# Optimization experiments

Measured on AMD Instinct MI355X. Metric: run time of the kernel, lower is better.

Reference implementation:

```python
import jax, jax.numpy as jnp
import numpy as np

B, N, D, V = 512, 200, 128, 100000

def setup_inputs() -> dict:
    key = jax.random.key(0)
    ks = jax.random.split(key, 13)
    s = 1.0 / np.sqrt(D)
    return {
        "x": jax.random.randint(ks[0], (B, N), 0, V),
        "A": jax.random.uniform(ks[1], (B, N, 2 * N), dtype=jnp.float32),
        "emb": jax.random.normal(ks[2], (V, D), dtype=jnp.float32) * s,
        "w_in": jax.random.normal(ks[3], (D, D), dtype=jnp.float32) * s,
        "b_in": jax.random.normal(ks[4], (D,), dtype=jnp.float32) * s,
        "w_out": jax.random.normal(ks[5], (D, D), dtype=jnp.float32) * s,
        "b_out": jax.random.normal(ks[6], (D,), dtype=jnp.float32) * s,
        "w_ih": jax.random.normal(ks[7], (3 * D, 2 * D), dtype=jnp.float32) * s,
        "b_ih": jax.random.normal(ks[8], (3 * D,), dtype=jnp.float32) * s,
        "w_hh": jax.random.normal(ks[9], (3 * D, D), dtype=jnp.float32) * s,
        "b_hh": jax.random.normal(ks[10], (3 * D,), dtype=jnp.float32) * s,
        "b_iah": jax.random.normal(ks[11], (D,), dtype=jnp.float32) * s,
        "b_oah": jax.random.normal(ks[12], (D,), dtype=jnp.float32) * s,
    }

def reference(x, A, emb, w_in, b_in, w_out, b_out, w_ih, b_ih, w_hh, b_hh, b_iah, b_oah):
    hidden = emb[x]                                   # [B, N, D]
    n = A.shape[1]
    # neighbor aggregation via in/out adjacency halves
    input_in = jnp.matmul(A[:, :, :n], hidden @ w_in.T + b_in) + b_iah    # [B, N, D]
    input_out = jnp.matmul(A[:, :, n:2 * n], hidden @ w_out.T + b_out) + b_oah
    inputs = jnp.concatenate([input_in, input_out], axis=2)               # [B, N, 2D]
    gi = inputs @ w_ih.T + b_ih                        # [B, N, 3D]
    gh = hidden @ w_hh.T + b_hh                        # [B, N, 3D]
    d = hidden.shape[-1]
    i_r, i_i, i_n = gi[..., :d], gi[..., d:2 * d], gi[..., 2 * d:]
    h_r, h_i, h_n = gh[..., :d], gh[..., d:2 * d], gh[..., 2 * d:]
    gate_input = jax.nn.sigmoid(i_i + h_i)
    gate_reset = jax.nn.sigmoid(i_r + h_r)
    gate_output = jnp.tanh(i_n + gate_reset * h_n)
    return gate_output + gate_input * (hidden - gate_output)
```

## Files before the change

### kernel.cpp

```cpp
#include <hip/hip_runtime.h>
#include <math.h>

#define BB 512
#define NN 200
#define DD 128
#define BNROWS (BB*NN)

typedef float f32x4 __attribute__((ext_vector_type(4)));
typedef short bf16x8 __attribute__((ext_vector_type(8)));
typedef unsigned short u16x4 __attribute__((ext_vector_type(4)));

#define MFMA16(a,b,c) __builtin_amdgcn_mfma_f32_16x16x32_bf16(a,b,c,0,0,0)

#define GLL(gp, lp) __builtin_amdgcn_global_load_lds( \
    (const __attribute__((address_space(1))) unsigned int*)(gp), \
    (__attribute__((address_space(3))) unsigned int*)(lp), 16, 0, 0)

#define KWAITV(S) asm volatile("s_waitcnt vmcnt(" S ")" ::: "memory")
#define KWAITL()  asm volatile("s_waitcnt lgkmcnt(0)" ::: "memory")
#define KBAR()    __builtin_amdgcn_s_barrier()
#define KSBAR()   __builtin_amdgcn_sched_barrier(0)

#define OFF_ZHI   ((size_t)0)
#define OFF_ZLO   (OFF_ZHI + (size_t)BNROWS*384*2)
#define OFF_HT    (OFF_ZLO + (size_t)BNROWS*256*2)
#define OFF_M1    (OFF_HT  + (size_t)BB*128*224*2)
#define OFF_M2    (OFF_M1  + (size_t)384*128*4)
#define OFF_WH    (OFF_M2  + (size_t)384*128*4)
#define OFF_WL    (OFF_WH  + (size_t)512*384*2)
#define OFF_CC    (OFF_WL  + (size_t)512*384*2)
#define OFF_U1V   (OFF_CC  + 512*4)
#define OFF_U2V   (OFF_U1V + 512*4)
#define OFF_U1    (OFF_U2V + 512*4)
#define OFF_U2    (OFF_U1  + 384*4)
#define OFF_C0    (OFF_U2  + 384*4)
#define OFF_RSI   (OFF_C0  + 384*4)
#define OFF_RSO   (OFF_RSI + (size_t)BNROWS*4)
#define WS_BYTES  (OFF_RSO + (size_t)BNROWS*4)

__device__ inline unsigned short f2bf(float x) {
  unsigned int u = __float_as_uint(x);
  unsigned int r = u + 0x7FFFu + ((u >> 16) & 1u);
  return (unsigned short)(r >> 16);
}
__device__ inline float bf2f(unsigned short h) {
  return __uint_as_float(((unsigned int)h) << 16);
}
__device__ inline float fsigmoid(float x) {
  return 1.f / (1.f + __expf(-x));
}
__device__ inline float ftanh(float x) {
  x = fminf(15.f, fmaxf(-15.f, x));
  float e = __expf(-2.f * x);
  return (1.f - e) / (1.f + e);
}

__global__ __launch_bounds__(128) void kprep(
    const float* __restrict__ w_ih, const float* __restrict__ w_in,
    const float* __restrict__ w_out, const float* __restrict__ b_in,
    const float* __restrict__ b_out, const float* __restrict__ b_iah,
    const float* __restrict__ b_oah, const float* __restrict__ b_ih,
    float* __restrict__ M1, float* __restrict__ M2,
    float* __restrict__ u1, float* __restrict__ u2, float* __restrict__ c0) {
  __shared__ float wrow[256];
  const int j = blockIdx.x;
  const int k = threadIdx.x;
  wrow[k]       = w_ih[(size_t)j * 256 + k];
  wrow[128 + k] = w_ih[(size_t)j * 256 + 128 + k];
  __syncthreads();
  float a1 = 0.f, a2 = 0.f;
  for (int t = 0; t < 128; ++t) {
    a1 = fmaf(wrow[t],       w_in[t * 128 + k],  a1);
    a2 = fmaf(wrow[128 + t], w_out[t * 128 + k], a2);
  }
  M1[j * 128 + k] = a1;
  M2[j * 128 + k] = a2;
  if (k == 0) {
    float s1 = 0.f, s2 = 0.f, s0 = 0.f;
    for (int t = 0; t < 128; ++t) {
      s1 = fmaf(wrow[t], b_in[t], s1);
      s2 = fmaf(wrow[128 + t], b_out[t], s2);
      s0 = fmaf(wrow[t], b_iah[t], s0);
      s0 = fmaf(wrow[128 + t], b_oah[t], s0);
    }
    u1[j] = s1; u2[j] = s2; c0[j] = s0 + b_ih[j];
  }
}

__global__ void wcat_build(const float* __restrict__ M1, const float* __restrict__ M2,
                           const float* __restrict__ w_hh, const float* __restrict__ b_hh,
                           const float* __restrict__ u1, const float* __restrict__ u2,
                           const float* __restrict__ c0,
                           unsigned short* __restrict__ Wh, unsigned short* __restrict__ Wl,
                           float* __restrict__ cc, float* __restrict__ u1v,
                           float* __restrict__ u2v) {
  int idx = blockIdx.x * 256 + threadIdx.x;
  if (idx >= 512 * 384) return;
  int jp = idx / 384, k = idx - jp * 384;
  int nh = jp >> 8, ng = (jp >> 7) & 1, t = (jp >> 4) & 7, q = jp & 15;
  int blk = t >> 1, s = t & 1;
  int c = nh * 64 + ng * 32 + s * 16 + q;
  int g = (blk <= 1) ? blk : 2;
  int j = g * 128 + c;
  float val;
  if (k < 128)      val = (blk == 3) ? 0.f : M1[j * 128 + k];
  else if (k < 256) val = (blk == 3) ? 0.f : M2[j * 128 + (k - 128)];
  else              val = (blk == 2) ? 0.f : w_hh[(size_t)j * 128 + (k - 256)];
  unsigned short h = f2bf(val);
  Wh[idx] = h;
  Wl[idx] = f2bf(val - bf2f(h));
  if (k == 0) {
    float ccv, a1, a2;
    if (blk == 0)      { ccv = c0[c] + b_hh[c];             a1 = u1[c];       a2 = u2[c]; }
    else if (blk == 1) { ccv = c0[128 + c] + b_hh[128 + c]; a1 = u1[128 + c]; a2 = u2[128 + c]; }
    else if (blk == 2) { ccv = c0[256 + c];                 a1 = u1[256 + c]; a2 = u2[256 + c]; }
    else               { ccv = b_hh[256 + c];               a1 = 0.f;         a2 = 0.f; }
    cc[jp] = ccv; u1v[jp] = a1; u2v[jp] = a2;
  }
}

__global__ __launch_bounds__(256) void k1_gather(
    const int* __restrict__ x, const float* __restrict__ emb,
    unsigned short* __restrict__ hT, unsigned short* __restrict__ Z_hi) {
  __shared__ float hid[32][132];
  const int t = threadIdx.x;
  const int b = blockIdx.x;
  const int m0 = blockIdx.y * 32;
  for (int i = t; i < 32 * 128; i += 256) {
    int r = i >> 7, c = i & 127;
    int m = m0 + r;
    int rowc = b * 200 + (m < 200 ? m : 199);
    float h = emb[(size_t)x[rowc] * 128 + c];
    hid[r][c] = h;
    if (m < 200) Z_hi[(size_t)(b * 200 + m) * 384 + 256 + c] = f2bf(h);
  }
  __syncthreads();
  {
    int c = t >> 1, half = t & 1;
    bf16x8 p0, p1;
    #pragma unroll
    for (int j = 0; j < 16; ++j) {
      int ml = half * 16 + j;
      bool valid = (m0 + ml) < 200;
      float fv = valid ? hid[ml][c] : 0.f;
      if (j < 8) p0[j] = (short)f2bf(fv);
      else       p1[j - 8] = (short)f2bf(fv);
    }
    size_t base = ((size_t)(b * 128 + c)) * 224 + m0 + half * 16;
    *(bf16x8*)&hT[base]     = p0;
    *(bf16x8*)&hT[base + 8] = p1;
  }
}

__global__ __launch_bounds__(256, 2) void k2_amm(
    const float* __restrict__ A, const unsigned short* __restrict__ hT,
    unsigned short* __restrict__ Z_hi, unsigned short* __restrict__ Z_lo,
    float* __restrict__ rs_in, float* __restrict__ rs_out) {
  __shared__ alignas(16) unsigned short Ainh[2][64][40];
  __shared__ alignas(16) unsigned short Ainl[2][64][40];
  __shared__ alignas(16) unsigned short Aouth[2][64][40];
  __shared__ alignas(16) unsigned short Aoutl[2][64][40];
  __shared__ alignas(16) unsigned short Bv[2][128][32];
  const int t = threadIdx.x;
  const int b = blockIdx.x;
  const int m0 = blockIdx.y * 64;
  const int wv = t >> 6, lane = t & 63;
  const int q = lane & 15, quad = lane >> 4;
  const int sel = wv >> 1, nh2 = wv & 1;
  const int lrow = lane >> 2, lseg = lane & 3;

  const int am = t >> 2, aseg = t & 3;
  const int gm = m0 + am;
  const bool mvalid = gm < 200;
  const float* arow = A + (size_t)(b * 200 + (mvalid ? gm : 199)) * 400;

  f32x4 acc[4][4];
  #pragma unroll
  for (int i = 0; i < 4; ++i)
    #pragma unroll
    for (int j = 0; j < 4; ++j) acc[i][j] = 0.f;
  float rsi = 0.f, rso = 0.f;

  #define AISSUE(K0, P0, P1, Q0, Q1) do {                                       \
    int kb_ = (K0) + aseg * 8;                                                  \
    int kc_ = (kb_ < 200) ? kb_ : 0;                                            \
    P0 = *(const f32x4*)(arow + kc_);                                           \
    P1 = *(const f32x4*)(arow + kc_ + 4);                                       \
    Q0 = *(const f32x4*)(arow + 200 + kc_);                                     \
    Q1 = *(const f32x4*)(arow + 200 + kc_ + 4);                                 \
  } while (0)

  #define STAGE_B(K0, BUF) do {                                                 \
    _Pragma("unroll")                                                           \
    for (int op_ = 0; op_ < 2; ++op_) {                                         \
      int j_ = wv * 32 + op_ * 16 + lrow;                                       \
      int c_ = ((j_ >> 6) << 6) + ((j_ & 15) << 2) + ((j_ >> 4) & 3);           \
      GLL(hT + ((size_t)(b * 128 + c_)) * 224 + (K0) + lseg * 8,                \
          &Bv[BUF][wv * 32 + op_ * 16][0]);                                     \
    }                                                                           \
  } while (0)

  #define ACONV(K0, BUF, P0, P1, Q0, Q1) do {                                   \
    bool kv_ = mvalid && ((K0) + aseg * 8 < 200);                               \
    float fin_[8], fot_[8];                                                     \
    fin_[0]=P0.x; fin_[1]=P0.y; fin_[2]=P0.z; fin_[3]=P0.w;                     \
    fin_[4]=P1.x; fin_[5]=P1.y; fin_[6]=P1.z; fin_[7]=P1.w;                     \
    fot_[0]=Q0.x; fot_[1]=Q0.y; fot_[2]=Q0.z; fot_[3]=Q0.w;                     \
    fot_[4]=Q1.x; fot_[5]=Q1.y; fot_[6]=Q1.z; fot_[7]=Q1.w;                     \
    bf16x8 ih_, il_, oh_, ol_;                                                  \
    _Pragma("unroll")                                                           \
    for (int e_ = 0; e_ < 8; ++e_) {                                            \
      float fi_ = kv_ ? fin_[e_] : 0.f;                                         \
      float fo_ = kv_ ? fot_[e_] : 0.f;                                         \
      rsi += fi_; rso += fo_;                                                   \
      unsigned short h1_ = f2bf(fi_);                                           \
      ih_[e_] = (short)h1_; il_[e_] = (short)f2bf(fi_ - bf2f(h1_));             \
      unsigned short h2_ = f2bf(fo_);                                           \
      oh_[e_] = (short)h2_; ol_[e_] = (short)f2bf(fo_ - bf2f(h2_));             \
    }                                                                           \
    *(bf16x8*)&Ainh[BUF][am][aseg * 8]  = ih_;                                  \
    *(bf16x8*)&Ainl[BUF][am][aseg * 8]  = il_;                                  \
    *(bf16x8*)&Aouth[BUF][am][aseg * 8] = oh_;                                  \
    *(bf16x8*)&Aoutl[BUF][am][aseg * 8] = ol_;                                  \
  } while (0)

  #define K2COMP(BUF) do {                                                      \
    const unsigned short (*Ath_)[40] = sel ? Aouth[BUF] : Ainh[BUF];            \
    const unsigned short (*Atl_)[40] = sel ? Aoutl[BUF] : Ainl[BUF];            \
    bf16x8 ah_[4], al_[4];                                                      \
    _Pragma("unroll")                                                           \
    for (int mt = 0; mt < 4; ++mt) {                                            \
      ah_[mt] = *(const bf16x8*)&Ath_[mt * 16 + q][quad * 8];                   \
      al_[mt] = *(const bf16x8*)&Atl_[mt * 16 + q][quad * 8];                   \
    }                                                                           \
    _Pragma("unroll")                                                           \
    for (int nt = 0; nt < 4; ++nt) {                                            \
      bf16x8 bb_ = *(const bf16x8*)&Bv[BUF][nh2 * 64 + nt * 16 + q][quad * 8];  \
      _Pragma("unroll")                                                         \
      for (int mt = 0; mt < 4; ++mt) {                                          \
        acc[mt][nt] = MFMA16(ah_[mt], bb_, acc[mt][nt]);                        \
        acc[mt][nt] = MFMA16(al_[mt], bb_, acc[mt][nt]);                        \
      }                                                                         \
    }                                                                           \
  } while (0)

  f32x4 cp0, cp1, cq0, cq1;
  AISSUE(0, cp0, cp1, cq0, cq1);
  STAGE_B(0, 0);
  int buf = 0;

  for (int k = 0; k < 6; ++k) {
    const int k0n = (k + 1) * 32;
    f32x4 np0, np1, nq0, nq1;
    AISSUE(k0n, np0, np1, nq0, nq1);
    STAGE_B(k0n, buf ^ 1);
    KWAITV("6"); KSBAR();
    ACONV(k * 32, buf, cp0, cp1, cq0, cq1);
    KWAITL(); KSBAR(); KBAR();
    K2COMP(buf);
    KBAR();
    cp0 = np0; cp1 = np1; cq0 = nq0; cq1 = nq1;
    buf ^= 1;
  }
  KWAITV("0"); KSBAR();
  ACONV(192, buf, cp0, cp1, cq0, cq1);
  KWAITL(); KSBAR(); KBAR();
  K2COMP(buf);

  const int colb = sel * 128 + nh2 * 64 + q * 4;
  #pragma unroll
  for (int mt = 0; mt < 4; ++mt) {
    #pragma unroll
    for (int r = 0; r < 4; ++r) {
      int m = m0 + mt * 16 + quad * 4 + r;
      if (m < 200) {
        u16x4 h4, l4;
        #pragma unroll
        for (int nt = 0; nt < 4; ++nt) {
          float v = acc[mt][nt][r];
          unsigned short hs = f2bf(v);
          h4[nt] = hs;
          l4[nt] = f2bf(v - bf2f(hs));
        }
        size_t row = (size_t)(b * 200 + m);
        *(u16x4*)&Z_hi[row * 384 + colb] = h4;
        *(u16x4*)&Z_lo[row * 256 + colb] = l4;
      }
    }
  }
  rsi += __shfl_xor(rsi, 1); rsi += __shfl_xor(rsi, 2);
  rso += __shfl_xor(rso, 1); rso += __shfl_xor(rso, 2);
  if (aseg == 0 && mvalid) {
    rs_in[(size_t)b * 200 + gm]  = rsi;
    rs_out[(size_t)b * 200 + gm] = rso;
  }
  #undef AISSUE
  #undef STAGE_B
  #undef ACONV
  #undef K2COMP
}

__global__ __launch_bounds__(256, 2) void k3_gates(
    const unsigned short* __restrict__ Z_hi, const unsigned short* __restrict__ Z_lo,
    const unsigned short* __restrict__ Wh, const unsigned short* __restrict__ Wl,
    const float* __restrict__ cc, const float* __restrict__ u1v,
    const float* __restrict__ u2v, const float* __restrict__ rs_in,
    const float* __restrict__ rs_out, float* __restrict__ out) {
  __shared__ alignas(16) unsigned short WhS[256][32];
  __shared__ alignas(16) unsigned short WlS[256][32];
  __shared__ alignas(16) unsigned short Ah[2][128][32];
  __shared__ alignas(16) unsigned short Al[2][128][32];
  const int t = threadIdx.x;
  const int w = t >> 6, lane = t & 63;
  const int q = lane & 15, quad = lane >> 4;
  const int mh = w >> 1, ng = w & 1;
  const int lrow = lane >> 2, lseg = lane & 3;
  const size_t rbase = (size_t)blockIdx.x * 128;
  const int nh = blockIdx.y;

  f32x4 acc[4][8];
  #pragma unroll
  for (int i = 0; i < 4; ++i)
    #pragma unroll
    for (int j = 0; j < 8; ++j) acc[i][j] = 0.f;

  #define STAGE_W(KC) do {                                                      \
    const int k0_ = (KC) * 32;                                                  \
    _Pragma("unroll")                                                           \
    for (int c_ = 0; c_ < 4; ++c_) {                                            \
      int j_ = w * 64 + c_ * 16;                                                \
      GLL(Wh + (size_t)(nh * 256 + j_ + lrow) * 384 + k0_ + lseg * 8,           \
          &WhS[j_][0]);                                                         \
    }                                                                           \
    _Pragma("unroll")                                                           \
    for (int c_ = 0; c_ < 4; ++c_) {                                            \
      int j_ = w * 64 + c_ * 16;                                                \
      GLL(Wl + (size_t)(nh * 256 + j_ + lrow) * 384 + k0_ + lseg * 8,           \
          &WlS[j_][0]);                                                         \
    }                                                                           \
  } while (0)

  #define STAGE_A1(KC, BUF) do {                                                \
    const int k0_ = (KC) * 32;                                                  \
    _Pragma("unroll")                                                           \
    for (int c_ = 0; c_ < 2; ++c_) {                                            \
      int m_ = w * 32 + c_ * 16;                                                \
      GLL(Z_hi + (rbase + m_ + lrow) * 384 + k0_ + lseg * 8, &Ah[BUF][m_][0]);  \
    }                                                                           \
    _Pragma("unroll")                                                           \
    for (int c_ = 0; c_ < 2; ++c_) {                                            \
      int m_ = w * 32 + c_ * 16;                                                \
      GLL(Z_lo + (rbase + m_ + lrow) * 256 + k0_ + lseg * 8, &Al[BUF][m_][0]);  \
    }                                                                           \
  } while (0)

  #define STAGE_A2(KC, BUF) do {                                                \
    const int k0_ = (KC) * 32;                                                  \
    _Pragma("unroll")                                                           \
    for (int c_ = 0; c_ < 2; ++c_) {                                            \
      int m_ = w * 32 + c_ * 16;                                                \
      GLL(Z_hi + (rbase + m_ + lrow) * 384 + k0_ + lseg * 8, &Ah[BUF][m_][0]);  \
    }                                                                           \
  } while (0)

  #define COMPUTE1(BUF) do {                                                    \
    bf16x8 ah_[4], al_[4];                                                      \
    _Pragma("unroll")                                                           \
    for (int mt = 0; mt < 4; ++mt) {                                            \
      ah_[mt] = *(const bf16x8*)&Ah[BUF][mh * 64 + mt * 16 + q][quad * 8];      \
      al_[mt] = *(const bf16x8*)&Al[BUF][mh * 64 + mt * 16 + q][quad * 8];      \
    }                                                                           \
    _Pragma("unroll")                                                           \
    for (int tt = 0; tt < 6; ++tt) {                                            \
      bf16x8 bh = *(const bf16x8*)&WhS[ng * 128 + tt * 16 + q][quad * 8];       \
      bf16x8 bl = *(const bf16x8*)&WlS[ng * 128 + tt * 16 + q][quad * 8];       \
      _Pragma("unroll")                                                         \
      for (int mt = 0; mt < 4; ++mt) {                                          \
        acc[mt][tt] = MFMA16(ah_[mt], bh, acc[mt][tt]);                         \
        acc[mt][tt] = MFMA16(ah_[mt], bl, acc[mt][tt]);                         \
        acc[mt][tt] = MFMA16(al_[mt], bh, acc[mt][tt]);                         \
      }                                                                         \
    }                                                                           \
  } while (0)

  #define COMPUTE2(BUF) do {                                                    \
    bf16x8 ah_[4];                                                              \
    _Pragma("unroll")                                                           \
    for (int mt = 0; mt < 4; ++mt)                                              \
      ah_[mt] = *(const bf16x8*)&Ah[BUF][mh * 64 + mt * 16 + q][quad * 8];      \
    _Pragma("unroll")                                                           \
    for (int ti = 0; ti < 6; ++ti) {                                            \
      const int tt = (ti < 4) ? ti : ti + 2;             \
      bf16x8 bh = *(const bf16x8*)&WhS[ng * 128 + tt * 16 + q][quad * 8];       \
      bf16x8 bl = *(const bf16x8*)&WlS[ng * 128 + tt * 16 + q][quad * 8];       \
      _Pragma("unroll")                                                         \
      for (int mt = 0; mt < 4; ++mt) {                                          \
        acc[mt][tt] = MFMA16(ah_[mt], bh, acc[mt][tt]);                         \
        acc[mt][tt] = MFMA16(ah_[mt], bl, acc[mt][tt]);                         \
      }                                                                         \
    }                                                                           \
  } while (0)

  STAGE_A1(0, 0);
  int buf = 0;
  #pragma unroll
  for (int kc = 0; kc < 7; ++kc) {
    STAGE_W(kc);
    STAGE_A1(kc + 1, buf ^ 1);
    KWAITV("4"); KSBAR(); KBAR();
    COMPUTE1(buf);
    KWAITL(); KSBAR(); KBAR();
    buf ^= 1;
  }
  {
    STAGE_W(7);
    STAGE_A2(8, buf ^ 1);
    KWAITV("2"); KSBAR(); KBAR();
    COMPUTE1(buf);
    KWAITL(); KSBAR(); KBAR();
    buf ^= 1;
  }
  #pragma unroll
  for (int kc = 8; kc < 11; ++kc) {
    STAGE_W(kc);
    STAGE_A2(kc + 1, buf ^ 1);
    KWAITV("2"); KSBAR(); KBAR();
    COMPUTE2(buf);
    KWAITL(); KSBAR(); KBAR();
    buf ^= 1;
  }
  {
    STAGE_W(11);
    KWAITV("0"); KSBAR(); KBAR();
    COMPUTE2(buf);
  }

  const int jb = nh * 256 + ng * 128;
  float cs[2][4], a1s[2][3], a2s[2][3];
  #pragma unroll
  for (int s = 0; s < 2; ++s) {
    #pragma unroll
    for (int gb = 0; gb < 4; ++gb) cs[s][gb] = cc[jb + (gb * 2 + s) * 16 + q];
    #pragma unroll
    for (int gb = 0; gb < 3; ++gb) {
      a1s[s][gb] = u1v[jb + (gb * 2 + s) * 16 + q];
      a2s[s][gb] = u2v[jb + (gb * 2 + s) * 16 + q];
    }
  }
  #pragma unroll
  for (int mt = 0; mt < 4; ++mt) {
    #pragma unroll
    for (int r = 0; r < 4; ++r) {
      size_t row = rbase + mh * 64 + mt * 16 + quad * 4 + r;
      float rin = rs_in[row], rot = rs_out[row];
      #pragma unroll
      for (int s = 0; s < 2; ++s) {
        int c = nh * 64 + ng * 32 + s * 16 + q;
        float sr  = acc[mt][0 + s][r] + cs[s][0] + rin * a1s[s][0] + rot * a2s[s][0];
        float si  = acc[mt][2 + s][r] + cs[s][1] + rin * a1s[s][1] + rot * a2s[s][1];
        float ani = acc[mt][4 + s][r] + cs[s][2] + rin * a1s[s][2] + rot * a2s[s][2];
        float anh = acc[mt][6 + s][r] + cs[s][3];
        float g_rs = fsigmoid(sr);
        float g_in = fsigmoid(si);
        float g_ot = ftanh(ani + g_rs * anh);
        float h = bf2f(Z_hi[row * 384 + 256 + c]);
        out[row * 128 + c] = g_ot + g_in * (h - g_ot);
      }
    }
  }
  #undef STAGE_W
  #undef STAGE_A1
  #undef STAGE_A2
  #undef COMPUTE1
  #undef COMPUTE2
}

extern "C" void kernel_launch(void* const* d_in, const int* in_sizes, int n_in,
                              void* d_out, int out_size, void* d_ws, size_t ws_size,
                              hipStream_t stream) {
  const int*   x     = (const int*)d_in[0];
  const float* A     = (const float*)d_in[1];
  const float* emb   = (const float*)d_in[2];
  const float* w_in  = (const float*)d_in[3];
  const float* b_in  = (const float*)d_in[4];
  const float* w_out = (const float*)d_in[5];
  const float* b_out = (const float*)d_in[6];
  const float* w_ih  = (const float*)d_in[7];
  const float* b_ih  = (const float*)d_in[8];
  const float* w_hh  = (const float*)d_in[9];
  const float* b_hh  = (const float*)d_in[10];
  const float* b_iah = (const float*)d_in[11];
  const float* b_oah = (const float*)d_in[12];
  float* out = (float*)d_out;
  char* ws = (char*)d_ws;

  if (ws_size < WS_BYTES) return;

  unsigned short* Z_hi = (unsigned short*)(ws + OFF_ZHI);
  unsigned short* Z_lo = (unsigned short*)(ws + OFF_ZLO);
  unsigned short* hT   = (unsigned short*)(ws + OFF_HT);
  float* M1 = (float*)(ws + OFF_M1);
  float* M2 = (float*)(ws + OFF_M2);
  unsigned short* Wh = (unsigned short*)(ws + OFF_WH);
  unsigned short* Wl = (unsigned short*)(ws + OFF_WL);
  float* ccv = (float*)(ws + OFF_CC);
  float* u1v = (float*)(ws + OFF_U1V);
  float* u2v = (float*)(ws + OFF_U2V);
  float* u1  = (float*)(ws + OFF_U1);
  float* u2  = (float*)(ws + OFF_U2);
  float* c0  = (float*)(ws + OFF_C0);
  float* rs_in  = (float*)(ws + OFF_RSI);
  float* rs_out = (float*)(ws + OFF_RSO);

  kprep<<<384, 128, 0, stream>>>(w_ih, w_in, w_out, b_in, b_out, b_iah, b_oah,
                                 b_ih, M1, M2, u1, u2, c0);
  wcat_build<<<(512 * 384 + 255) / 256, 256, 0, stream>>>(M1, M2, w_hh, b_hh,
                                                          u1, u2, c0, Wh, Wl,
                                                          ccv, u1v, u2v);
  dim3 g1(BB, 7);
  k1_gather<<<g1, 256, 0, stream>>>(x, emb, hT, Z_hi);
  dim3 g2(BB, 4);
  k2_amm<<<g2, 256, 0, stream>>>(A, hT, Z_hi, Z_lo, rs_in, rs_out);
  dim3 g3(BNROWS / 128, 2);
  k3_gates<<<g3, 256, 0, stream>>>(Z_hi, Z_lo, Wh, Wl, ccv, u1v, u2v,
                                   rs_in, rs_out, out);
}
```

Measured before the change: 503.9 us.

## Double-buffer and trim weight staging in gate kernel; swizzle B tile in AMM

The gate kernel now double-buffers its weight tiles, prefetching the next K chunk alongside the activation tile instead of loading weights synchronously each step. It stages only the 192 weight rows each phase actually uses (skipping unused gate blocks), with separate row maps for the two phases and adjusted vmcnt waits. The AMM kernel XOR-swizzles the LDS column segment of the B tile to reduce bank conflicts on the MFMA operand reads. The cost is more LDS per block and more complex index arithmetic, which could lower occupancy or break correctness if the waitcnt values are wrong.

```diff
diff --git a/kernel.cpp b/kernel.cpp
--- a/kernel.cpp
+++ b/kernel.cpp
@@ -168,6 +168,8 @@
   const int q = lane & 15, quad = lane >> 4;
   const int sel = wv >> 1, nh2 = wv & 1;
   const int lrow = lane >> 2, lseg = lane & 3;
+  const int sx8 = (lseg ^ ((lrow >> 1) & 3)) * 8;
+  const int qs8 = (quad ^ ((q >> 1) & 3)) * 8;
 
   const int am = t >> 2, aseg = t & 3;
   const int gm = m0 + am;
@@ -195,7 +197,7 @@
     for (int op_ = 0; op_ < 2; ++op_) {                                         \
       int j_ = wv * 32 + op_ * 16 + lrow;                                       \
       int c_ = ((j_ >> 6) << 6) + ((j_ & 15) << 2) + ((j_ >> 4) & 3);           \
-      GLL(hT + ((size_t)(b * 128 + c_)) * 224 + (K0) + lseg * 8,                \
+      GLL(hT + ((size_t)(b * 128 + c_)) * 224 + (K0) + sx8,                     \
           &Bv[BUF][wv * 32 + op_ * 16][0]);                                     \
     }                                                                           \
   } while (0)
@@ -235,7 +237,7 @@
     }                                                                           \
     _Pragma("unroll")                                                           \
     for (int nt = 0; nt < 4; ++nt) {                                            \
-      bf16x8 bb_ = *(const bf16x8*)&Bv[BUF][nh2 * 64 + nt * 16 + q][quad * 8];  \
+      bf16x8 bb_ = *(const bf16x8*)&Bv[BUF][nh2 * 64 + nt * 16 + q][qs8];       \
       _Pragma("unroll")                                                         \
       for (int mt = 0; mt < 4; ++mt) {                                          \
         acc[mt][nt] = MFMA16(ah_[mt], bb_, acc[mt][nt]);                        \
@@ -306,8 +308,8 @@
     const float* __restrict__ cc, const float* __restrict__ u1v,
     const float* __restrict__ u2v, const float* __restrict__ rs_in,
     const float* __restrict__ rs_out, float* __restrict__ out) {
-  __shared__ alignas(16) unsigned short WhS[256][32];
-  __shared__ alignas(16) unsigned short WlS[256][32];
+  __shared__ alignas(16) unsigned short WhS[2][192][32];
+  __shared__ alignas(16) unsigned short WlS[2][192][32];
   __shared__ alignas(16) unsigned short Ah[2][128][32];
   __shared__ alignas(16) unsigned short Al[2][128][32];
   const int t = threadIdx.x;
@@ -324,19 +326,41 @@
     #pragma unroll
     for (int j = 0; j < 8; ++j) acc[i][j] = 0.f;
 
-  #define STAGE_W(KC) do {                                                      \
+  #define STAGE_W1(KC, BUF) do {                                                \
     const int k0_ = (KC) * 32;                                                  \
     _Pragma("unroll")                                                           \
-    for (int c_ = 0; c_ < 4; ++c_) {                                            \
-      int j_ = w * 64 + c_ * 16;                                                \
-      GLL(Wh + (size_t)(nh * 256 + j_ + lrow) * 384 + k0_ + lseg * 8,           \
-          &WhS[j_][0]);                                                         \
-    }                                                                           \
-    _Pragma("unroll")                                                           \
-    for (int c_ = 0; c_ < 4; ++c_) {                                            \
-      int j_ = w * 64 + c_ * 16;                                                \
-      GLL(Wl + (size_t)(nh * 256 + j_ + lrow) * 384 + k0_ + lseg * 8,           \
-          &WlS[j_][0]);                                                         \
+    for (int c_ = 0; c_ < 3; ++c_) {                                            \
+      int j0_ = w * 48 + c_ * 16;                                               \
+      int hp_ = (j0_ >= 96) ? 1 : 0;                                            \
+      int gr_ = nh * 256 + hp_ * 128 + (j0_ - hp_ * 96) + lrow;                 \
+      GLL(Wh + (size_t)gr_ * 384 + k0_ + lseg * 8, &WhS[BUF][j0_][0]);          \
+    }                                                                           \
+    _Pragma("unroll")                                                           \
+    for (int c_ = 0; c_ < 3; ++c_) {                                            \
+      int j0_ = w * 48 + c_ * 16;                                               \
+      int hp_ = (j0_ >= 96) ? 1 : 0;                                            \
+      int gr_ = nh * 256 + hp_ * 128 + (j0_ - hp_ * 96) + lrow;                 \
+      GLL(Wl + (size_t)gr_ * 384 + k0_ + lseg * 8, &WlS[BUF][j0_][0]);          \
+    }                                                                           \
+  } while (0)
+
+  #define STAGE_W2(KC, BUF) do {                                                \
+    const int k0_ = (KC) * 32;                                                  \
+    _Pragma("unroll")                                                           \
+    for (int c_ = 0; c_ < 3; ++c_) {                                            \
+      int j0_ = w * 48 + c_ * 16;                                               \
+      int hp_ = (j0_ >= 96) ? 1 : 0;                                            \
+      int jc_ = j0_ - hp_ * 96;                                                 \
+      int gr_ = nh * 256 + hp_ * 128 + (jc_ < 64 ? jc_ : jc_ + 32) + lrow;      \
+      GLL(Wh + (size_t)gr_ * 384 + k0_ + lseg * 8, &WhS[BUF][j0_][0]);          \
+    }                                                                           \
+    _Pragma("unroll")                                                           \
+    for (int c_ = 0; c_ < 3; ++c_) {                                            \
+      int j0_ = w * 48 + c_ * 16;                                               \
+      int hp_ = (j0_ >= 96) ? 1 : 0;                                            \
+      int jc_ = j0_ - hp_ * 96;                                                 \
+      int gr_ = nh * 256 + hp_ * 128 + (jc_ < 64 ? jc_ : jc_ + 32) + lrow;      \
+      GLL(Wl + (size_t)gr_ * 384 + k0_ + lseg * 8, &WlS[BUF][j0_][0]);          \
     }                                                                           \
   } while (0)
 
@@ -372,8 +396,8 @@
     }                                                                           \
     _Pragma("unroll")                                                           \
     for (int tt = 0; tt < 6; ++tt) {                                            \
-      bf16x8 bh = *(const bf16x8*)&WhS[ng * 128 + tt * 16 + q][quad * 8];       \
-      bf16x8 bl = *(const bf16x8*)&WlS[ng * 128 + tt * 16 + q][quad * 8];       \
+      bf16x8 bh = *(const bf16x8*)&WhS[BUF][ng * 96 + tt * 16 + q][quad * 8];   \
+      bf16x8 bl = *(const bf16x8*)&WlS[BUF][ng * 96 + tt * 16 + q][quad * 8];   \
       _Pragma("unroll")                                                         \
       for (int mt = 0; mt < 4; ++mt) {                                          \
         acc[mt][tt] = MFMA16(ah_[mt], bh, acc[mt][tt]);                         \
@@ -391,8 +415,9 @@
     _Pragma("unroll")                                                           \
     for (int ti = 0; ti < 6; ++ti) {                                            \
       const int tt = (ti < 4) ? ti : ti + 2;             \
-      bf16x8 bh = *(const bf16x8*)&WhS[ng * 128 + tt * 16 + q][quad * 8];       \
-      bf16x8 bl = *(const bf16x8*)&WlS[ng * 128 + tt * 16 + q][quad * 8];       \
+      const int wr = ng * 96 + ((tt < 4) ? tt * 16 : 64 + (tt - 6) * 16) + q;   \
+      bf16x8 bh = *(const bf16x8*)&WhS[BUF][wr][quad * 8];                      \
+      bf16x8 bl = *(const bf16x8*)&WlS[BUF][wr][quad * 8];                      \
       _Pragma("unroll")                                                         \
       for (int mt = 0; mt < 4; ++mt) {                                          \
         acc[mt][tt] = MFMA16(ah_[mt], bh, acc[mt][tt]);                         \
@@ -401,36 +426,36 @@
     }                                                                           \
   } while (0)
 
+  STAGE_W1(0, 0);
   STAGE_A1(0, 0);
   int buf = 0;
   #pragma unroll
   for (int kc = 0; kc < 7; ++kc) {
-    STAGE_W(kc);
+    STAGE_W1(kc + 1, buf ^ 1);
     STAGE_A1(kc + 1, buf ^ 1);
-    KWAITV("4"); KSBAR(); KBAR();
+    KWAITV("10"); KSBAR(); KBAR();
     COMPUTE1(buf);
     KWAITL(); KSBAR(); KBAR();
     buf ^= 1;
   }
   {
-    STAGE_W(7);
+    STAGE_W2(8, buf ^ 1);
     STAGE_A2(8, buf ^ 1);
-    KWAITV("2"); KSBAR(); KBAR();
+    KWAITV("8"); KSBAR(); KBAR();
     COMPUTE1(buf);
     KWAITL(); KSBAR(); KBAR();
     buf ^= 1;
   }
   #pragma unroll
   for (int kc = 8; kc < 11; ++kc) {
-    STAGE_W(kc);
+    STAGE_W2(kc + 1, buf ^ 1);
     STAGE_A2(kc + 1, buf ^ 1);
-    KWAITV("2"); KSBAR(); KBAR();
+    KWAITV("8"); KSBAR(); KBAR();
     COMPUTE2(buf);
     KWAITL(); KSBAR(); KBAR();
     buf ^= 1;
   }
   {
-    STAGE_W(11);
     KWAITV("0"); KSBAR(); KBAR();
     COMPUTE2(buf);
   }
@@ -468,7 +493,8 @@
       }
     }
   }
-  #undef STAGE_W
+  #undef STAGE_W1
+  #undef STAGE_W2
   #undef STAGE_A1
   #undef STAGE_A2
   #undef COMPUTE1
```

Measured after the change: 495.9 us. Within noise of the previous version (-1.6%).
